# Performance work log

Hardware: AMD Instinct MI355X
Metric: run time of the kernel (lower is better)

The kernel has to match this reference:

```python
import jax, jax.numpy as jnp
import numpy as np

S, N, F, E, H = 64, 1000, 64, 128, 2  # seq_len, nodes/graph, node_dim, emb_dim, heads
DEG = 8
C = E // H  # per-head channels


def setup_inputs() -> dict:
    key = jax.random.key(0)
    ks = jax.random.split(key, 16)
    Ntot = S * N
    Eg = N * DEG
    src = jax.random.randint(ks[0], (S, Eg), 0, N)
    dst = jax.random.randint(ks[1], (S, Eg), 0, N)
    off = (jnp.arange(S) * N)[:, None]
    edge_index = jnp.stack([(src + off).reshape(-1), (dst + off).reshape(-1)]).astype(jnp.int32)
    nfm = jax.random.normal(ks[2], (Ntot, F), jnp.float32)
    reachable = jax.random.uniform(ks[3], (S, N)) > 0.2
    reachable = reachable.at[:, 0].set(True)  # ensure each row has a reachable node
    h0 = jnp.zeros((N, E), jnp.float32)
    c0 = jnp.zeros((N, E), jnp.float32)

    def lin(k, i, o):
        return (jax.random.normal(k, (i, o), jnp.float32) / np.sqrt(i)).astype(jnp.float32)

    return dict(
        nfm=nfm, edge_index=edge_index, reachable=reachable, h0=h0, c0=c0,
        gat_W1=lin(ks[4], F, E), gat_b1=jnp.zeros((E,), jnp.float32),
        gat_att1=(jax.random.normal(ks[5], (H, C), jnp.float32) / np.sqrt(C)).astype(jnp.float32),
        gat_bias1=jnp.zeros((E,), jnp.float32),
        gat_W=(jax.random.normal(ks[6], (4, E, E), jnp.float32) / np.sqrt(E)).astype(jnp.float32),
        gat_b=jnp.zeros((4, E), jnp.float32),
        gat_att=(jax.random.normal(ks[7], (4, H, C), jnp.float32) / np.sqrt(C)).astype(jnp.float32),
        gat_bias=jnp.zeros((4, E), jnp.float32),
        lstm_Wih=(jax.random.normal(ks[8], (4 * E, E), jnp.float32) / np.sqrt(E)).astype(jnp.float32),
        lstm_Whh=(jax.random.normal(ks[9], (4 * E, E), jnp.float32) / np.sqrt(E)).astype(jnp.float32),
        lstm_bih=jnp.zeros((4 * E,), jnp.float32), lstm_bhh=jnp.zeros((4 * E,), jnp.float32),
        th6_W=lin(ks[10], E, E), th6_b=jnp.zeros((E,), jnp.float32),
        th7_W=lin(ks[11], E, E), th7_b=jnp.zeros((E,), jnp.float32),
        th5_W=lin(ks[12], 2 * E, 1), th5_b=jnp.zeros((1,), jnp.float32),
    )


def _gat_layer(x, src, dst, W, b, att, bias, Ntot):
    # GATv2Conv, share_weights=True: x_l == x_r = lin(x)
    Hh, Ch = att.shape
    xl = (x @ W + b).reshape(-1, Hh, Ch)                 # [Ntot,H,C]
    e = jax.nn.leaky_relu(xl[src] + xl[dst], 0.2)        # [Etot,H,C]
    logit = jnp.einsum('ehc,hc->eh', e, att)             # [Etot,H]
    m = jax.ops.segment_max(logit, dst, num_segments=Ntot)
    a = jnp.exp(logit - m[dst])                          # segment-stable softmax
    denom = jax.ops.segment_sum(a, dst, num_segments=Ntot)
    alpha = a / denom[dst]
    out = jax.ops.segment_sum(xl[src] * alpha[:, :, None], dst, num_segments=Ntot)
    return out.reshape(-1, Hh * Ch) + bias               # concat heads + bias


def _forward(nfm, edge_index, reachable, h0, c0, gat_W1, gat_b1, gat_att1, gat_bias1,
             gat_W, gat_b, gat_att, gat_bias, lstm_Wih, lstm_Whh, lstm_bih, lstm_bhh,
             th6_W, th6_b, th7_W, th7_b, th5_W, th5_b):
    Ntot = nfm.shape[0]
    loops = jnp.arange(Ntot, dtype=edge_index.dtype)     # add_self_loops=True
    src = jnp.concatenate([edge_index[0], loops])
    dst = jnp.concatenate([edge_index[1], loops])

    x = jax.nn.relu(_gat_layer(nfm, src, dst, gat_W1, gat_b1, gat_att1, gat_bias1, Ntot))
    for i in range(4):  # layers 2..5; no activation after last
        x = _gat_layer(x, src, dst, gat_W[i], gat_b[i], gat_att[i], gat_bias[i], Ntot)
        if i < 3:
            x = jax.nn.relu(x)

    mu = x.reshape(S, N, E)                              # [seq, batch(=nodes), emb]

    def step(carry, xt):
        h, c = carry
        g = xt @ lstm_Wih.T + lstm_bih + h @ lstm_Whh.T + lstm_bhh
        i_, f_, gg, o_ = jnp.split(g, 4, axis=-1)        # torch gate order i,f,g,o
        c = jax.nn.sigmoid(f_) * c + jax.nn.sigmoid(i_) * jnp.tanh(gg)
        h = jax.nn.sigmoid(o_) * jnp.tanh(c)
        return (h, c), h

    (hT, cT), mu = jax.lax.scan(step, (h0, c0), mu)      # mu: [S,N,E]

    meanpool = mu.mean(axis=1, keepdims=True)            # [S,1,E]
    gs = meanpool @ th6_W + th6_b
    la = mu @ th7_W + th7_b
    rep = jax.nn.relu(jnp.concatenate([jnp.broadcast_to(gs, la.shape), la], axis=-1))
    logits = (rep @ th5_W)[..., 0] + th5_b               # [S,N]
    logits = jnp.where(reachable, logits, -jnp.inf)
    prob = jax.nn.softmax(logits, axis=1)
    return prob, hT, cT


def reference(nfm, edge_index, reachable, h0, c0, gat_W1, gat_b1, gat_att1, gat_bias1,
              gat_W, gat_b, gat_att, gat_bias, lstm_Wih, lstm_Whh, lstm_bih, lstm_bhh,
              th6_W, th6_b, th7_W, th7_b, th5_W, th5_b):
    return _forward(nfm, edge_index, reachable, h0, c0, gat_W1, gat_b1, gat_att1, gat_bias1,
                    gat_W, gat_b, gat_att, gat_bias, lstm_Wih, lstm_Whh, lstm_bih, lstm_bhh,
                    th6_W, th6_b, th7_W, th7_b, th5_W, th5_b)
```

## Files before the change

### kernel.cpp

```cpp
#include <hip/hip_runtime.h>
#include <hip/hip_bf16.h>

#define SQ   64
#define NN   1000
#define NT   64000
#define EE   128
#define EG   512000
#define ET   576000

#define WS_XA      0ull
#define WS_XB      33000000ull
#define WS_ROWPTR  66000000ull
#define WS_CURSOR  66300000ull
#define WS_SRCS    66600000ull
#define WS_INCL    69000000ull
#define WS_BSUM    69300000ull
#define WS_BOFF    69302048ull
#define WS_MODE    69304096ull
#define WS_WQA     70000000ull
#define WS_WQB     70262144ull
#define WS_AS      70600000ull
#define WS_LOGIT2  70700000ull
#define WS2_XC     33000000ull
#define WS2_BFRAG  164100000ull
#define WS2_GHI    164300000ull
#define WS2_GLO    164650000ull
#define WS2_B512   165000000ull
#define WS2_MODE   165010000ull
#define WS2_AS     165020000ull
#define WS2_LOGIT2 165100000ull
#define WS2_NEED   165360000ull
#define G_W1    0
#define G_WL    8192
#define G_PROJ  73728
#define G_W7    139264

typedef __attribute__((ext_vector_type(8))) short short8;
typedef __attribute__((ext_vector_type(4))) float f32x4;

__device__ __forceinline__ float rdlane(float v, int l) {
    return __int_as_float(__builtin_amdgcn_readlane(__float_as_int(v), l));
}
__device__ __forceinline__ float sigm(float x) { return 1.0f / (1.0f + __expf(-x)); }
__device__ __forceinline__ float tanh_f(float x) {
    x = fminf(fmaxf(x, -30.0f), 30.0f);
    float e = __expf(2.0f * x);
    return (e - 1.0f) / (e + 1.0f);
}
__device__ __forceinline__ float tanh2(float x) {
    return 2.0f / (1.0f + __expf(-2.0f * x)) - 1.0f;
}
__device__ __forceinline__ ushort f2bf(float x) {
    unsigned u = __float_as_uint(x);
    unsigned r = (u + 0x7FFFu + ((u >> 16) & 1u)) >> 16;
    return (ushort)r;
}
__device__ __forceinline__ float bf2f(ushort h) {
    return __uint_as_float(((unsigned)h) << 16);
}

__global__ void detect_mode_k(const unsigned char* __restrict__ p, int* __restrict__ mode) {
    __shared__ int f0, f3;
    const int t = threadIdx.x;
    if (t == 0) { f0 = 0; f3 = 0; }
    __syncthreads();
    int l0 = 0, l3 = 0;
    for (int i = t; i < 16000; i += 256) {
        if (p[4 * i])     l0 = 1;
        if (p[4 * i + 3]) l3 = 1;
    }
    if (l0) atomicOr(&f0, 1);
    if (l3) atomicOr(&f3, 1);
    __syncthreads();
    if (t == 0) {
        int m;
        if (f0 && f3)      m = 1;
        else if (f0)       m = 0;
        else               m = 2;
        *mode = m;
    }
}

__global__ void zero_ints_k(int* __restrict__ p, int n) {
    int i = blockIdx.x * 256 + threadIdx.x;
    if (i < n) p[i] = 0;
}
__global__ void hist_k(const int* __restrict__ ei, int* __restrict__ deg) {
    int e = blockIdx.x * 256 + threadIdx.x;
    if (e < ET) {
        int d = (e < EG) ? ei[EG + e] : (e - EG);
        atomicAdd(deg + d, 1);
    }
}
__global__ void scan1_k(const int* __restrict__ deg, int* __restrict__ incl, int* __restrict__ bsum) {
    __shared__ int sh[256];
    const int t = threadIdx.x;
    const int i = blockIdx.x * 256 + t;
    sh[t] = deg[i];
    __syncthreads();
    for (int o = 1; o < 256; o <<= 1) {
        int add = (t >= o) ? sh[t - o] : 0;
        __syncthreads();
        sh[t] += add;
        __syncthreads();
    }
    incl[i] = sh[t];
    if (t == 255) bsum[blockIdx.x] = sh[255];
}
__global__ void scan2_k(const int* __restrict__ bsum, int* __restrict__ boff) {
    __shared__ int sh[256];
    const int t = threadIdx.x;
    int v = (t < 250) ? bsum[t] : 0;
    sh[t] = v;
    __syncthreads();
    for (int o = 1; o < 256; o <<= 1) {
        int add = (t >= o) ? sh[t - o] : 0;
        __syncthreads();
        sh[t] += add;
        __syncthreads();
    }
    if (t < 250) boff[t] = sh[t] - v;
}
__global__ void scan3_k(const int* __restrict__ incl, const int* __restrict__ boff,
                        int* __restrict__ rowptr, int* __restrict__ cursor_deg) {
    const int i = blockIdx.x * 256 + threadIdx.x;
    int total = incl[i] + boff[blockIdx.x];
    int excl  = total - cursor_deg[i];
    rowptr[i] = excl;
    cursor_deg[i] = excl;
    if (i == NT - 1) rowptr[NT] = total;
}
__global__ void fill_k(const int* __restrict__ ei, int* __restrict__ cursor, int* __restrict__ srcs) {
    int e = blockIdx.x * 256 + threadIdx.x;
    if (e < ET) {
        int s_, d_;
        if (e < EG) { s_ = ei[e]; d_ = ei[EG + e]; }
        else        { s_ = e - EG; d_ = s_; }
        int p = atomicAdd(cursor + d_, 1);
        srcs[p] = s_;
    }
}

__global__ void build_gfrag_k(const float* __restrict__ src, const int ks, const int ns,
                              const int K, ushort* __restrict__ dhi, ushort* __restrict__ dlo,
                              const int total) {
    int id = blockIdx.x * 256 + threadIdx.x;
    if (id < total) {
        int j = id & 7, lane = (id >> 3) & 63;
        int f = id >> 9;
        int KT = K >> 5;
        int nt = f / KT, kt = f - nt * KT;
        int n = nt * 16 + (lane & 15);
        int k = kt * 32 + ((lane >> 4) << 3) + j;
        float v = src[(size_t)k * ks + (size_t)n * ns];
        ushort h = f2bf(v);
        dhi[id] = h;
        dlo[id] = f2bf(v - bf2f(h));
    }
}
__global__ void bias512_k(const float* __restrict__ bih, const float* __restrict__ bhh,
                          float* __restrict__ b512) {
    int i = blockIdx.x * 256 + threadIdx.x;
    if (i < 512) b512[i] = bih[i] + bhh[i];
}

template <int KT>
__global__ __launch_bounds__(256) void gemm_mf(
    const float* __restrict__ x, const ushort* __restrict__ bhi,
    const ushort* __restrict__ blo, const float* __restrict__ bias,
    float* __restrict__ out, const int ldout)
{
    constexpr int K = KT * 32;
    __shared__ __align__(16) ushort ahi_s[KT * 4 * 64 * 8];
    __shared__ __align__(16) ushort alo_s[KT * 4 * 64 * 8];
    const int t = threadIdx.x;
    const int w = t >> 6, lane = t & 63;
    const int quad = lane >> 4, col = lane & 15;
    const int row0 = blockIdx.x * 64;
    const int col0 = blockIdx.y * 128;

    {
        const int r  = t >> 2;
        const int kc = (t & 3) * (K / 4);
        const int rw = r >> 4, rcol = r & 15;
        const float* xr = x + (size_t)(row0 + r) * K + kc;
#pragma unroll
        for (int k = 0; k < K / 4; k += 4) {
            const int ch = kc + k;
            const int idx = (((ch >> 5) * 4 + rw) * 64 + ((ch >> 3) & 3) * 16 + rcol) * 8
                            + (ch & 7);
            float4 v = *(const float4*)(xr + k);
            ushort h0_ = f2bf(v.x), h1_ = f2bf(v.y), h2_ = f2bf(v.z), h3_ = f2bf(v.w);
            ushort l0_ = f2bf(v.x - bf2f(h0_)), l1_ = f2bf(v.y - bf2f(h1_));
            ushort l2_ = f2bf(v.z - bf2f(h2_)), l3_ = f2bf(v.w - bf2f(h3_));
            *(uint2*)(ahi_s + idx) = make_uint2((uint)h0_ | ((uint)h1_ << 16),
                                                (uint)h2_ | ((uint)h3_ << 16));
            *(uint2*)(alo_s + idx) = make_uint2((uint)l0_ | ((uint)l1_ << 16),
                                                (uint)l2_ | ((uint)l3_ << 16));
        }
    }
    __syncthreads();

    short8 ah[KT], al[KT];
#pragma unroll
    for (int kt = 0; kt < KT; kt++) {
        const int off = ((kt * 4 + w) * 64 + lane) * 8;
        ah[kt] = *(const short8*)(ahi_s + off);
        al[kt] = *(const short8*)(alo_s + off);
    }

    f32x4 acc[8];
#pragma unroll
    for (int q = 0; q < 8; q++) acc[q] = (f32x4){0.f, 0.f, 0.f, 0.f};

#pragma unroll
    for (int q = 0; q < 8; q++) {
#pragma unroll
        for (int kt = 0; kt < KT; kt++) {
            const int f = ((((col0 >> 4) + q) * KT + kt) * 64 + lane) * 8;
            short8 bh = *(const short8*)(bhi + f);
            short8 bl = *(const short8*)(blo + f);
            acc[q] = __builtin_amdgcn_mfma_f32_16x16x32_bf16(ah[kt], bh, acc[q], 0, 0, 0);
            acc[q] = __builtin_amdgcn_mfma_f32_16x16x32_bf16(al[kt], bh, acc[q], 0, 0, 0);
            acc[q] = __builtin_amdgcn_mfma_f32_16x16x32_bf16(ah[kt], bl, acc[q], 0, 0, 0);
        }
    }

#pragma unroll
    for (int q = 0; q < 8; q++) {
        float bv = bias[col0 + q * 16 + col];
#pragma unroll
        for (int r = 0; r < 4; r++) {
            out[(size_t)(row0 + w * 16 + quad * 4 + r) * ldout + col0 + q * 16 + col]
                = acc[q][r] + bv;
        }
    }
}

template <int K>
__global__ __launch_bounds__(256) void gemm3(
    const float* __restrict__ x, const float* __restrict__ W,
    const float* __restrict__ b, float* __restrict__ out)
{
    __shared__ float Wsh[64 * 128];
    __shared__ float xT[64][132];
    const int t = threadIdx.x;
    const int row0 = blockIdx.x * 128;
    const int cg = t & 15;
    const int rg = t >> 4;
    float4 acc[8][2];
#pragma unroll
    for (int r = 0; r < 8; r++) {
        acc[r][0] = make_float4(0.f, 0.f, 0.f, 0.f);
        acc[r][1] = make_float4(0.f, 0.f, 0.f, 0.f);
    }
    for (int k0 = 0; k0 < K; k0 += 64) {
        for (int i = t * 4; i < 64 * 128; i += 1024)
            *(float4*)(Wsh + i) = *(const float4*)(W + (size_t)k0 * 128 + i);
        for (int i = t * 4; i < 128 * 64; i += 1024) {
            int r = i >> 6, k = i & 63;
            float4 v = *(const float4*)(x + (size_t)(row0 + r) * K + k0 + k);
            xT[k + 0][r] = v.x; xT[k + 1][r] = v.y;
            xT[k + 2][r] = v.z; xT[k + 3][r] = v.w;
        }
        __syncthreads();
#pragma unroll 2
        for (int k = 0; k < 64; k++) {
            float4 w0 = *(const float4*)(Wsh + k * 128 + cg * 8);
            float4 w1 = *(const float4*)(Wsh + k * 128 + cg * 8 + 4);
            float4 x0 = *(const float4*)(&xT[k][rg * 8]);
            float4 x1 = *(const float4*)(&xT[k][rg * 8 + 4]);
            float xv[8] = {x0.x, x0.y, x0.z, x0.w, x1.x, x1.y, x1.z, x1.w};
#pragma unroll
            for (int r = 0; r < 8; r++) {
                acc[r][0].x += xv[r] * w0.x; acc[r][0].y += xv[r] * w0.y;
                acc[r][0].z += xv[r] * w0.z; acc[r][0].w += xv[r] * w0.w;
                acc[r][1].x += xv[r] * w1.x; acc[r][1].y += xv[r] * w1.y;
                acc[r][1].z += xv[r] * w1.z; acc[r][1].w += xv[r] * w1.w;
            }
        }
        __syncthreads();
    }
    float4 bv0 = *(const float4*)(b + cg * 8);
    float4 bv1 = *(const float4*)(b + cg * 8 + 4);
#pragma unroll
    for (int r = 0; r < 8; r++) {
        float4 o0, o1;
        o0.x = acc[r][0].x + bv0.x; o0.y = acc[r][0].y + bv0.y;
        o0.z = acc[r][0].z + bv0.z; o0.w = acc[r][0].w + bv0.w;
        o1.x = acc[r][1].x + bv1.x; o1.y = acc[r][1].y + bv1.y;
        o1.z = acc[r][1].z + bv1.z; o1.w = acc[r][1].w + bv1.w;
        float* op = out + (size_t)(row0 + rg * 8 + r) * 128 + cg * 8;
        *(float4*)(op) = o0;
        *(float4*)(op + 4) = o1;
    }
}

__global__ __launch_bounds__(256) void gat_fused_k(
    const float* __restrict__ xl, const int* __restrict__ rowptr,
    const int* __restrict__ srcs, const float* __restrict__ att,
    const float* __restrict__ bias, float* __restrict__ out, const int do_relu)
{
    const int lane = threadIdx.x & 63;
    const int q = lane & 31;
    const int h = lane >> 5;
    const int b = blockIdx.x;
    const int g = b & 7;
    const int j = b >> 3;
    const int jq = j / 250;
    const int jj = j - jq * 250;
    const int s = g + 8 * jq;
    const int n = s * NN + jj * 4 + (threadIdx.x >> 6);

    const float4 a4 = *(const float4*)(att + q * 4);
    const float4 xd = *(const float4*)(xl + (size_t)n * 128 + q * 4);
    const int i0 = rowptr[n], i1 = rowptr[n + 1];

    float m = -1e30f, d = 0.f;
    float ax = 0.f, ay = 0.f, az = 0.f, aw = 0.f;

    int i = i0 + h;
    int sv = (i < i1) ? srcs[i] : 0;
    for (int base = i0; base < i1; base += 2) {
        const bool valid = (i < i1);
        const int svn = (i + 2 < i1) ? srcs[i + 2] : 0;
        const float4 xs = *(const float4*)(xl + (size_t)sv * 128 + q * 4);
        float u0 = xs.x + xd.x, u1 = xs.y + xd.y;
        float u2 = xs.z + xd.z, u3 = xs.w + xd.w;
        float p;
        p  = a4.x * fmaxf(u0, 0.2f * u0);
        p += a4.y * fmaxf(u1, 0.2f * u1);
        p += a4.z * fmaxf(u2, 0.2f * u2);
        p += a4.w * fmaxf(u3, 0.2f * u3);
        p += __shfl_xor(p, 1);
        p += __shfl_xor(p, 2);
        p += __shfl_xor(p, 4);
        p += __shfl_xor(p, 8);
        float mn = fmaxf(m, valid ? p : -1e30f);
        float sc = __expf(m - mn);
        float wgt = valid ? __expf(p - mn) : 0.f;
        d  = d  * sc + wgt;
        ax = ax * sc + wgt * xs.x;
        ay = ay * sc + wgt * xs.y;
        az = az * sc + wgt * xs.z;
        aw = aw * sc + wgt * xs.w;
        m = mn;
        sv = svn;
        i += 2;
    }

    float m2 = __shfl_xor(m, 32);
    float d2 = __shfl_xor(d, 32);
    float bx = __shfl_xor(ax, 32);
    float by = __shfl_xor(ay, 32);
    float bz = __shfl_xor(az, 32);
    float bw = __shfl_xor(aw, 32);
    float mm = fmaxf(m, m2);
    float s1 = __expf(m - mm), s2 = __expf(m2 - mm);
    float den = d * s1 + d2 * s2;
    float inv = 1.f / den;
    float4 bv = *(const float4*)(bias + q * 4);
    float ox = (ax * s1 + bx * s2) * inv + bv.x;
    float oy = (ay * s1 + by * s2) * inv + bv.y;
    float oz = (az * s1 + bz * s2) * inv + bv.z;
    float ow = (aw * s1 + bw * s2) * inv + bv.w;
    if (do_relu) {
        ox = fmaxf(ox, 0.f); oy = fmaxf(oy, 0.f);
        oz = fmaxf(oz, 0.f); ow = fmaxf(ow, 0.f);
    }
    if (lane < 32)
        *(float4*)(out + (size_t)n * 128 + q * 4) = make_float4(ox, oy, oz, ow);
}

__global__ void build_wq_k(const float* __restrict__ Wih, const float* __restrict__ Whh,
                           float4* __restrict__ WQa, float4* __restrict__ WQb) {
    int id = blockIdx.x * 256 + threadIdx.x;
    if (id < 64 * 256) {
        int kp = id >> 8, t = id & 255;
        int j1 = t, j2 = t + 256;
        WQa[id] = make_float4(Wih[(size_t)j1 * 128 + 2 * kp], Whh[(size_t)j1 * 128 + 2 * kp],
                              Wih[(size_t)j1 * 128 + 2 * kp + 1], Whh[(size_t)j1 * 128 + 2 * kp + 1]);
        WQb[id] = make_float4(Wih[(size_t)j2 * 128 + 2 * kp], Whh[(size_t)j2 * 128 + 2 * kp],
                              Wih[(size_t)j2 * 128 + 2 * kp + 1], Whh[(size_t)j2 * 128 + 2 * kp + 1]);
    }
}

__global__ void build_bfrag_k(const float* __restrict__ Whh, ushort* __restrict__ Bfrag) {
    int id = blockIdx.x * 256 + threadIdx.x;
    if (id < 65536) {
        int j = id & 7, lane = (id >> 3) & 63, kt = (id >> 9) & 3, tile = id >> 11;
        int gate = tile * 16 + (lane & 15);
        int k = kt * 32 + ((lane >> 4) << 3) + j;
        Bfrag[id] = f2bf(Whh[(size_t)gate * 128 + k]);
    }
}

#define LSTM_GROUP(buf, gbase)                                                     \
    _Pragma("unroll")                                                              \
    for (int i_ = 0; i_ < 4; i_++) {                                               \
        const int kp_ = (gbase) * 4 + i_;                                          \
        const float4 qa_ = buf[i_];                                                \
        const float4 qb_ = buf[4 + i_];                                            \
        _Pragma("unroll")                                                          \
        for (int n_ = 0; n_ < 4; n_++) {                                           \
            const float sx0_ = rdlane(xr[n_].x, kp_);                              \
            const float sh0_ = rdlane(hr[n_].x, kp_);                              \
            const float sx1_ = rdlane(xr[n_].y, kp_);                              \
            const float sh1_ = rdlane(hr[n_].y, kp_);                              \
            acc1[n_] += sx0_ * qa_.x + sh0_ * qa_.y + sx1_ * qa_.z + sh1_ * qa_.w; \
            acc2[n_] += sx0_ * qb_.x + sh0_ * qb_.y + sx1_ * qb_.z + sh1_ * qb_.w; \
        }                                                                          \
    }

__global__ __launch_bounds__(256, 1) void lstm_k(
    float* __restrict__ mu, const float4* __restrict__ WQa, const float4* __restrict__ WQb,
    const float* __restrict__ bih, const float* __restrict__ bhh,
    const float* __restrict__ h0, const float* __restrict__ c0,
    float* __restrict__ hT, float* __restrict__ cT)
{
    const int t = threadIdx.x, lane = t & 63;
    const int n0 = blockIdx.x * 4;
    __shared__ float hsh[4][128];
    __shared__ float gsh[4][512];
    const float b1 = bih[t] + bhh[t];
    const float b2 = bih[t + 256] + bhh[t + 256];
    float creg[2];
#pragma unroll
    for (int q = 0; q < 2; q++) {
        int id = t + 256 * q;
        creg[q] = c0[(size_t)(n0 + (id >> 7)) * 128 + (id & 127)];
    }
    for (int i = t; i < 512; i += 256)
        hsh[i >> 7][i & 127] = h0[(size_t)(n0 + (i >> 7)) * 128 + (i & 127)];

    const float4* pA = WQa + t;
    const float4* pB = WQb + t;

    float2 xr[4], xnx[4];
#pragma unroll
    for (int n = 0; n < 4; n++)
        xr[n] = *(const float2*)(mu + (size_t)n0 * 128 + n * 128 + lane * 2);
    __syncthreads();

    for (int s = 0; s < SQ; s++) {
        float* xrow = mu + ((size_t)s * NN + n0) * 128;
        float2 hr[4];
#pragma unroll
        for (int n = 0; n < 4; n++) hr[n] = *(const float2*)(&hsh[n][lane * 2]);

        float4 bufA[8], bufB[8];
#pragma unroll
        for (int i = 0; i < 4; i++) { bufA[i] = pA[i * 256]; bufA[4 + i] = pB[i * 256]; }

        if (s + 1 < SQ) {
            const float* xrow2 = mu + ((size_t)(s + 1) * NN + n0) * 128;
#pragma unroll
            for (int n = 0; n < 4; n++) xnx[n] = *(const float2*)(xrow2 + n * 128 + lane * 2);
        }

        float acc1[4], acc2[4];
#pragma unroll
        for (int n = 0; n < 4; n++) { acc1[n] = b1; acc2[n] = b2; }

        for (int g = 0; g < 16; g += 2) {
#pragma unroll
            for (int i = 0; i < 4; i++) {
                bufB[i]     = pA[((g + 1) * 4 + i) * 256];
                bufB[4 + i] = pB[((g + 1) * 4 + i) * 256];
            }
            LSTM_GROUP(bufA, g)
            if (g < 14) {
#pragma unroll
                for (int i = 0; i < 4; i++) {
                    bufA[i]     = pA[((g + 2) * 4 + i) * 256];
                    bufA[4 + i] = pB[((g + 2) * 4 + i) * 256];
                }
            }
            LSTM_GROUP(bufB, g + 1)
        }

#pragma unroll
        for (int n = 0; n < 4; n++) { gsh[n][t] = acc1[n]; gsh[n][t + 256] = acc2[n]; }
        __syncthreads();
#pragma unroll
        for (int q = 0; q < 2; q++) {
            int id = t + 256 * q;
            int n = id >> 7, e = id & 127;
            float iv = gsh[n][e], fv = gsh[n][128 + e];
            float gv = gsh[n][256 + e], ov = gsh[n][384 + e];
            float c = sigm(fv) * creg[q] + sigm(iv) * tanh_f(gv);
            float h = sigm(ov) * tanh_f(c);
            creg[q] = c;
            hsh[n][e] = h;
            xrow[n * 128 + e] = h;
            if (s == SQ - 1) {
                hT[(size_t)(n0 + n) * 128 + e] = h;
                cT[(size_t)(n0 + n) * 128 + e] = c;
            }
        }
#pragma unroll
        for (int n = 0; n < 4; n++) xr[n] = xnx[n];
        __syncthreads();
    }
}

__global__ __launch_bounds__(512, 2) void lstm10_k(
    float* __restrict__ mu, const float* __restrict__ xC,
    const ushort* __restrict__ Bfrag,
    const float* __restrict__ h0, const float* __restrict__ c0,
    float* __restrict__ hT, float* __restrict__ cT)
{
    const int t = threadIdx.x;
    const int w = t >> 6, lane = t & 63;
    const int quad = lane >> 4;
    const int n0 = blockIdx.x * 4;
    const int enode = t >> 7;
    const int ech   = t & 127;

    __shared__ __align__(16) ushort hP[2][2][2048];
    __shared__ float gsh[4][512];

    short8 bf[4][4];
#pragma unroll
    for (int g4 = 0; g4 < 4; g4++)
#pragma unroll
        for (int kt = 0; kt < 4; kt++) {
            int tile = g4 * 8 + w;
            bf[g4][kt] = *(const short8*)(Bfrag + (((tile * 4 + kt) * 64 + lane) << 3));
        }

    const int epkt = ech >> 5, epqd = (ech >> 3) & 3, epj = ech & 7;
    const int epidx = epkt * 512 + (epqd * 16 + enode) * 8 + epj;

    for (int i = t; i < 2 * 2 * 2048; i += 512) ((ushort*)hP)[i] = 0;
    __syncthreads();
    {
        float v = h0[(size_t)(n0 + enode) * 128 + ech];
        ushort hh = f2bf(v), hl = f2bf(v - bf2f(hh));
        hP[0][0][epidx] = hh; hP[0][1][epidx] = hl;
        hP[1][0][epidx] = hh; hP[1][1][epidx] = hl;
    }
    float cst = c0[(size_t)(n0 + enode) * 128 + ech];

    float xcr[4], xcn[4];
#pragma unroll
    for (int g4 = 0; g4 < 4; g4++)
        xcr[g4] = xC[((size_t)(n0 + enode)) * 512 + g4 * 128 + ech];
    __syncthreads();

    int p = 0;
    for (int s = 0; s < SQ; s++) {
        if (s + 1 < SQ) {
            const float* xn = xC + ((size_t)(s + 1) * NN + n0 + enode) * 512;
#pragma unroll
            for (int g4 = 0; g4 < 4; g4++)
                xcn[g4] = xn[g4 * 128 + ech];
        }

        short8 ahi[4], alo[4];
#pragma unroll
        for (int kt = 0; kt < 4; kt++) {
            ahi[kt] = *(const short8*)(&hP[p][0][kt * 512 + lane * 8]);
            alo[kt] = *(const short8*)(&hP[p][1][kt * 512 + lane * 8]);
        }

        f32x4 acc[4];
#pragma unroll
        for (int g4 = 0; g4 < 4; g4++) acc[g4] = (f32x4){0.f, 0.f, 0.f, 0.f};
#pragma unroll
        for (int kt = 0; kt < 4; kt++) {
#pragma unroll
            for (int g4 = 0; g4 < 4; g4++)
                acc[g4] = __builtin_amdgcn_mfma_f32_16x16x32_bf16(ahi[kt], bf[g4][kt], acc[g4], 0, 0, 0);
#pragma unroll
            for (int g4 = 0; g4 < 4; g4++)
                acc[g4] = __builtin_amdgcn_mfma_f32_16x16x32_bf16(alo[kt], bf[g4][kt], acc[g4], 0, 0, 0);
        }

        if (quad == 0) {
            const int col = lane & 15;
#pragma unroll
            for (int g4 = 0; g4 < 4; g4++)
#pragma unroll
                for (int r = 0; r < 4; r++)
                    gsh[r][(g4 * 8 + w) * 16 + col] = acc[g4][r];
        }
        __syncthreads();

        {
            float iv = gsh[enode][0 * 128 + ech] + xcr[0];
            float fv = gsh[enode][1 * 128 + ech] + xcr[1];
            float gv = gsh[enode][2 * 128 + ech] + xcr[2];
            float ov = gsh[enode][3 * 128 + ech] + xcr[3];
            float c = sigm(fv) * cst + sigm(iv) * tanh2(gv);
            float h = sigm(ov) * tanh2(c);
            cst = c;
            const int pn = p ^ 1;
            ushort hh = f2bf(h);
            hP[pn][0][epidx] = hh;
            hP[pn][1][epidx] = f2bf(h - bf2f(hh));
            mu[((size_t)s * NN + n0 + enode) * 128 + ech] = h;
            if (s == SQ - 1) {
                hT[(size_t)(n0 + enode) * 128 + ech] = h;
                cT[(size_t)(n0 + enode) * 128 + ech] = c;
            }
            p = pn;
        }
#pragma unroll
        for (int g4 = 0; g4 < 4; g4++) xcr[g4] = xcn[g4];
        __syncthreads();
    }
}

__global__ __launch_bounds__(256) void meanpool_gs_k(
    const float* __restrict__ mu, const float* __restrict__ W6,
    const float* __restrict__ b6, const float* __restrict__ w5,
    float* __restrict__ A)
{
    const int s = blockIdx.x, t = threadIdx.x;
    const int ch = t & 127, half = t >> 7;
    __shared__ float mp[128];
    __shared__ float red[256];
    float acc = 0.f;
    for (int n = half * 500; n < (half + 1) * 500; n++)
        acc += mu[((size_t)s * NN + n) * 128 + ch];
    red[t] = acc;
    __syncthreads();
    if (t < 128) mp[t] = (red[t] + red[t + 128]) * 0.001f;
    __syncthreads();
    float g = 0.f;
    if (t < 128) {
        g = b6[t];
        for (int k = 0; k < 128; k++) g += mp[k] * W6[(size_t)k * 128 + t];
        g = fmaxf(g, 0.f) * w5[t];
    }
    red[t] = g;
    __syncthreads();
    for (int o = 128; o > 0; o >>= 1) {
        if (t < o) red[t] += red[t + o];
        __syncthreads();
    }
    if (t == 0) A[s] = red[0];
}

__global__ __launch_bounds__(256) void rowdot_k(
    const float* __restrict__ la, const float* __restrict__ w5,
    const float* __restrict__ b5, const float* __restrict__ A,
    float* __restrict__ out)
{
    const int lane = threadIdx.x & 63;
    const int row = blockIdx.x * 4 + (threadIdx.x >> 6);
    float2 v = *(const float2*)(la + (size_t)row * 128 + lane * 2);
    float2 w = *(const float2*)(w5 + 128 + lane * 2);
    float x = fmaxf(v.x, 0.f) * w.x + fmaxf(v.y, 0.f) * w.y;
#pragma unroll
    for (int o = 32; o; o >>= 1) x += __shfl_down(x, o);
    if (lane == 0) out[row] = x + A[row / NN] + b5[0];
}

__device__ __forceinline__ bool reach_at(const void* reach, int mode, int idx) {
    if (mode == 0) return ((const int*)reach)[idx] != 0;
    if (mode == 1) return ((const unsigned char*)reach)[idx] != 0;
    return ((const float*)reach)[idx] != 0.f;
}
__global__ __launch_bounds__(256) void softmax_k(
    const float* __restrict__ lg, const void* __restrict__ reach,
    const int* __restrict__ mode, float* __restrict__ prob)
{
    const int s = blockIdx.x, t = threadIdx.x;
    const int m = *mode;
    __shared__ float red[256];
    float mx = -1e30f;
    for (int i = t; i < NN; i += 256) {
        int idx = s * NN + i;
        if (reach_at(reach, m, idx)) mx = fmaxf(mx, lg[idx]);
    }
    red[t] = mx;
    __syncthreads();
    for (int o = 128; o; o >>= 1) {
        if (t < o) red[t] = fmaxf(red[t], red[t + o]);
        __syncthreads();
    }
    mx = red[0];
    __syncthreads();
    float sum = 0.f;
    for (int i = t; i < NN; i += 256) {
        int idx = s * NN + i;
        float v = reach_at(reach, m, idx) ? __expf(lg[idx] - mx) : 0.f;
        prob[idx] = v;
        sum += v;
    }
    red[t] = sum;
    __syncthreads();
    for (int o = 128; o; o >>= 1) {
        if (t < o) red[t] += red[t + o];
        __syncthreads();
    }
    float inv = 1.f / red[0];
    for (int i = t; i < NN; i += 256) prob[s * NN + i] *= inv;
}

extern "C" void kernel_launch(void* const* d_in, const int* in_sizes, int n_in,
                              void* d_out, int out_size, void* d_ws, size_t ws_size,
                              hipStream_t stream) {
    const float* nfm   = (const float*)d_in[0];
    const int*   ei    = (const int*)d_in[1];
    const void*  reach = d_in[2];
    const float* h0    = (const float*)d_in[3];
    const float* c0    = (const float*)d_in[4];
    const float* W1    = (const float*)d_in[5];
    const float* b1    = (const float*)d_in[6];
    const float* att1  = (const float*)d_in[7];
    const float* bias1 = (const float*)d_in[8];
    const float* Wl    = (const float*)d_in[9];
    const float* bl    = (const float*)d_in[10];
    const float* attl  = (const float*)d_in[11];
    const float* biasl = (const float*)d_in[12];
    const float* Wih   = (const float*)d_in[13];
    const float* Whh   = (const float*)d_in[14];
    const float* bih   = (const float*)d_in[15];
    const float* bhh   = (const float*)d_in[16];
    const float* W6    = (const float*)d_in[17];
    const float* b6    = (const float*)d_in[18];
    const float* W7    = (const float*)d_in[19];
    const float* b7    = (const float*)d_in[20];
    const float* w5    = (const float*)d_in[21];
    const float* b5    = (const float*)d_in[22];

    char* ws = (char*)d_ws;
    const bool bigws = (ws_size >= WS2_NEED);

    float*  xA     = (float*)(ws + WS_XA);
    float*  xB     = (float*)(ws + WS_XB);
    int*    rowptr = (int*)(ws + WS_ROWPTR);
    int*    cursor = (int*)(ws + WS_CURSOR);
    int*    srcs   = (int*)(ws + WS_SRCS);
    int*    incl   = (int*)(ws + WS_INCL);
    int*    bsum   = (int*)(ws + WS_BSUM);
    int*    boff   = (int*)(ws + WS_BOFF);
    int*    modep  = bigws ? (int*)(ws + WS2_MODE)     : (int*)(ws + WS_MODE);
    float*  As     = bigws ? (float*)(ws + WS2_AS)     : (float*)(ws + WS_AS);
    float*  logit2 = bigws ? (float*)(ws + WS2_LOGIT2) : (float*)(ws + WS_LOGIT2);
    float*  xC     = (float*)(ws + WS2_XC);
    ushort* Bfrag  = (ushort*)(ws + WS2_BFRAG);
    ushort* ghi    = (ushort*)(ws + WS2_GHI);
    ushort* glo    = (ushort*)(ws + WS2_GLO);
    float*  b512   = (float*)(ws + WS2_B512);
    float4* WQa    = (float4*)(ws + WS_WQA);
    float4* WQb    = (float4*)(ws + WS_WQB);

    float* prob = (float*)d_out;
    float* hT   = (float*)d_out + 64000;
    float* cT   = (float*)d_out + 192000;

    detect_mode_k<<<1, 256, 0, stream>>>((const unsigned char*)reach, modep);
    zero_ints_k<<<250, 256, 0, stream>>>(cursor, NT);
    hist_k<<<2250, 256, 0, stream>>>(ei, cursor);
    scan1_k<<<250, 256, 0, stream>>>(cursor, incl, bsum);
    scan2_k<<<1, 256, 0, stream>>>(bsum, boff);
    scan3_k<<<250, 256, 0, stream>>>(incl, boff, rowptr, cursor);
    fill_k<<<2250, 256, 0, stream>>>(ei, cursor, srcs);
    if (bigws) {
        build_bfrag_k<<<256, 256, 0, stream>>>(Whh, Bfrag);
        bias512_k<<<2, 256, 0, stream>>>(bih, bhh, b512);
        build_gfrag_k<<<32, 256, 0, stream>>>(W1, 128, 1, 64, ghi + G_W1, glo + G_W1, 8192);
        for (int i = 0; i < 4; i++)
            build_gfrag_k<<<64, 256, 0, stream>>>(Wl + (size_t)i * 16384, 128, 1, 128,
                                                  ghi + G_WL + i * 16384, glo + G_WL + i * 16384, 16384);
        build_gfrag_k<<<256, 256, 0, stream>>>(Wih, 1, 128, 128, ghi + G_PROJ, glo + G_PROJ, 65536);
        build_gfrag_k<<<64, 256, 0, stream>>>(W7, 128, 1, 128, ghi + G_W7, glo + G_W7, 16384);
    } else {
        build_wq_k<<<64, 256, 0, stream>>>(Wih, Whh, WQa, WQb);
    }

    for (int l = 0; l < 5; l++) {
        if (bigws) {
            if (l == 0)
                gemm_mf<2><<<dim3(1000, 1), 256, 0, stream>>>(nfm, ghi + G_W1, glo + G_W1, b1, xB, 128);
            else
                gemm_mf<4><<<dim3(1000, 1), 256, 0, stream>>>(xA, ghi + G_WL + (l - 1) * 16384,
                                                              glo + G_WL + (l - 1) * 16384,
                                                              bl + (l - 1) * 128, xB, 128);
        } else {
            if (l == 0)
                gemm3<64><<<500, 256, 0, stream>>>(nfm, W1, b1, xB);
            else
                gemm3<128><<<500, 256, 0, stream>>>(xA, Wl + (size_t)(l - 1) * 128 * 128,
                                                    bl + (l - 1) * 128, xB);
        }
        const float* att  = (l == 0) ? att1  : attl  + (l - 1) * 128;
        const float* bias = (l == 0) ? bias1 : biasl + (l - 1) * 128;
        gat_fused_k<<<16000, 256, 0, stream>>>(xB, rowptr, srcs, att, bias, xA,
                                               (l < 4) ? 1 : 0);
    }

    if (bigws) {
        gemm_mf<4><<<dim3(1000, 4), 256, 0, stream>>>(xA, ghi + G_PROJ, glo + G_PROJ, b512, xC, 512);
        lstm10_k<<<250, 512, 0, stream>>>(xA, xC, Bfrag, h0, c0, hT, cT);
    } else {
        lstm_k<<<250, 256, 0, stream>>>(xA, WQa, WQb, bih, bhh, h0, c0, hT, cT);
    }

    meanpool_gs_k<<<64, 256, 0, stream>>>(xA, W6, b6, w5, As);
    if (bigws)
        gemm_mf<4><<<dim3(1000, 1), 256, 0, stream>>>(xA, ghi + G_W7, glo + G_W7, b7, xB, 128);
    else
        gemm3<128><<<500, 256, 0, stream>>>(xA, W7, b7, xB);
    rowdot_k<<<16000, 256, 0, stream>>>(xB, w5, b5, As, logit2);
    softmax_k<<<64, 256, 0, stream>>>(logit2, reach, modep, prob);
}
```

Before: 692.9 us.

## Merge weight-prep launches, dual-stream GAT edge loop, pad LSTM h buffer

Nine small weight-preparation kernels become one launch that picks its task from the block index, which cuts launch overhead. The GAT aggregation loop now runs two independent online-softmax streams per half-wave, with two edges' source loads in flight and merged at the end, to hide gather latency. The LSTM kernel keeps h in a padded row-major shared buffer (stride 136) instead of a fragment-ordered layout, which changes the LDS access pattern and zero-pads the unused rows. The cost is more registers in the GAT kernel and a more irregular LDS read pattern in the LSTM.

```diff
diff --git a/kernel.cpp b/kernel.cpp
--- a/kernel.cpp
+++ b/kernel.cpp
@@ -141,10 +141,10 @@
     }
 }
 
-__global__ void build_gfrag_k(const float* __restrict__ src, const int ks, const int ns,
-                              const int K, ushort* __restrict__ dhi, ushort* __restrict__ dlo,
-                              const int total) {
-    int id = blockIdx.x * 256 + threadIdx.x;
+__device__ __forceinline__ void gfrag_dev(const float* __restrict__ src, const int ks,
+                                          const int ns, const int K,
+                                          ushort* __restrict__ dhi, ushort* __restrict__ dlo,
+                                          const int total, const int id) {
     if (id < total) {
         int j = id & 7, lane = (id >> 3) & 63;
         int f = id >> 9;
@@ -158,10 +158,34 @@
         dlo[id] = f2bf(v - bf2f(h));
     }
 }
-__global__ void bias512_k(const float* __restrict__ bih, const float* __restrict__ bhh,
-                          float* __restrict__ b512) {
-    int i = blockIdx.x * 256 + threadIdx.x;
-    if (i < 512) b512[i] = bih[i] + bhh[i];
+__global__ void build_all_k(const float* __restrict__ Whh, const float* __restrict__ bih,
+                            const float* __restrict__ bhh, const float* __restrict__ W1,
+                            const float* __restrict__ Wl, const float* __restrict__ Wih,
+                            const float* __restrict__ W7, ushort* __restrict__ Bfrag,
+                            float* __restrict__ b512, ushort* __restrict__ ghi,
+                            ushort* __restrict__ glo) {
+    const int b = blockIdx.x, t = threadIdx.x;
+    if (b < 256) {
+        int id = b * 256 + t;
+        int j = id & 7, lane = (id >> 3) & 63, kt = (id >> 9) & 3, tile = id >> 11;
+        int gate = tile * 16 + (lane & 15);
+        int k = kt * 32 + ((lane >> 4) << 3) + j;
+        Bfrag[id] = f2bf(Whh[(size_t)gate * 128 + k]);
+    } else if (b < 258) {
+        int i = (b - 256) * 256 + t;
+        if (i < 512) b512[i] = bih[i] + bhh[i];
+    } else if (b < 290) {
+        gfrag_dev(W1, 128, 1, 64, ghi + G_W1, glo + G_W1, 8192, (b - 258) * 256 + t);
+    } else if (b < 546) {
+        int bb = b - 290;
+        int i = bb >> 6;
+        gfrag_dev(Wl + (size_t)i * 16384, 128, 1, 128,
+                  ghi + G_WL + i * 16384, glo + G_WL + i * 16384, 16384, (bb & 63) * 256 + t);
+    } else if (b < 802) {
+        gfrag_dev(Wih, 1, 128, 128, ghi + G_PROJ, glo + G_PROJ, 65536, (b - 546) * 256 + t);
+    } else {
+        gfrag_dev(W7, 128, 1, 128, ghi + G_W7, glo + G_W7, 16384, (b - 802) * 256 + t);
+    }
 }
 
 template <int KT>
@@ -316,38 +340,63 @@
     const float4 xd = *(const float4*)(xl + (size_t)n * 128 + q * 4);
     const int i0 = rowptr[n], i1 = rowptr[n + 1];
 
-    float m = -1e30f, d = 0.f;
-    float ax = 0.f, ay = 0.f, az = 0.f, aw = 0.f;
-
-    int i = i0 + h;
-    int sv = (i < i1) ? srcs[i] : 0;
-    for (int base = i0; base < i1; base += 2) {
-        const bool valid = (i < i1);
-        const int svn = (i + 2 < i1) ? srcs[i + 2] : 0;
-        const float4 xs = *(const float4*)(xl + (size_t)sv * 128 + q * 4);
-        float u0 = xs.x + xd.x, u1 = xs.y + xd.y;
-        float u2 = xs.z + xd.z, u3 = xs.w + xd.w;
-        float p;
-        p  = a4.x * fmaxf(u0, 0.2f * u0);
-        p += a4.y * fmaxf(u1, 0.2f * u1);
-        p += a4.z * fmaxf(u2, 0.2f * u2);
-        p += a4.w * fmaxf(u3, 0.2f * u3);
-        p += __shfl_xor(p, 1);
-        p += __shfl_xor(p, 2);
-        p += __shfl_xor(p, 4);
-        p += __shfl_xor(p, 8);
-        float mn = fmaxf(m, valid ? p : -1e30f);
-        float sc = __expf(m - mn);
-        float wgt = valid ? __expf(p - mn) : 0.f;
-        d  = d  * sc + wgt;
-        ax = ax * sc + wgt * xs.x;
-        ay = ay * sc + wgt * xs.y;
-        az = az * sc + wgt * xs.z;
-        aw = aw * sc + wgt * xs.w;
-        m = mn;
-        sv = svn;
-        i += 2;
-    }
+    float mA = -1e30f, dA = 0.f, axA = 0.f, ayA = 0.f, azA = 0.f, awA = 0.f;
+    float mB = -1e30f, dB = 0.f, axB = 0.f, ayB = 0.f, azB = 0.f, awB = 0.f;
+
+    int iA = i0 + h, iB = i0 + h + 2;
+    int svA = (iA < i1) ? srcs[iA] : 0;
+    int svB = (iB < i1) ? srcs[iB] : 0;
+    float4 xsA = *(const float4*)(xl + (size_t)svA * 128 + q * 4);
+    float4 xsB = *(const float4*)(xl + (size_t)svB * 128 + q * 4);
+
+    for (int base = i0; base < i1; base += 4) {
+        const bool vA = (iA < i1), vB = (iB < i1);
+        const int svA2 = (iA + 4 < i1) ? srcs[iA + 4] : 0;
+        const int svB2 = (iB + 4 < i1) ? srcs[iB + 4] : 0;
+        const float4 xA2 = *(const float4*)(xl + (size_t)svA2 * 128 + q * 4);
+        const float4 xB2 = *(const float4*)(xl + (size_t)svB2 * 128 + q * 4);
+
+        float uA0 = xsA.x + xd.x, uA1 = xsA.y + xd.y;
+        float uA2 = xsA.z + xd.z, uA3 = xsA.w + xd.w;
+        float uB0 = xsB.x + xd.x, uB1 = xsB.y + xd.y;
+        float uB2 = xsB.z + xd.z, uB3 = xsB.w + xd.w;
+        float pA, pB;
+        pA  = a4.x * fmaxf(uA0, 0.2f * uA0);
+        pA += a4.y * fmaxf(uA1, 0.2f * uA1);
+        pA += a4.z * fmaxf(uA2, 0.2f * uA2);
+        pA += a4.w * fmaxf(uA3, 0.2f * uA3);
+        pB  = a4.x * fmaxf(uB0, 0.2f * uB0);
+        pB += a4.y * fmaxf(uB1, 0.2f * uB1);
+        pB += a4.z * fmaxf(uB2, 0.2f * uB2);
+        pB += a4.w * fmaxf(uB3, 0.2f * uB3);
+        pA += __shfl_xor(pA, 1);   pB += __shfl_xor(pB, 1);
+        pA += __shfl_xor(pA, 2);   pB += __shfl_xor(pB, 2);
+        pA += __shfl_xor(pA, 4);   pB += __shfl_xor(pB, 4);
+        pA += __shfl_xor(pA, 8);   pB += __shfl_xor(pB, 8);
+
+        float mnA = fmaxf(mA, vA ? pA : -1e30f);
+        float mnB = fmaxf(mB, vB ? pB : -1e30f);
+        float scA = __expf(mA - mnA), scB = __expf(mB - mnB);
+        float wA = vA ? __expf(pA - mnA) : 0.f;
+        float wB = vB ? __expf(pB - mnB) : 0.f;
+        dA  = dA  * scA + wA;          dB  = dB  * scB + wB;
+        axA = axA * scA + wA * xsA.x;  axB = axB * scB + wB * xsB.x;
+        ayA = ayA * scA + wA * xsA.y;  ayB = ayB * scB + wB * xsB.y;
+        azA = azA * scA + wA * xsA.z;  azB = azB * scB + wB * xsB.z;
+        awA = awA * scA + wA * xsA.w;  awB = awB * scB + wB * xsB.w;
+        mA = mnA; mB = mnB;
+        xsA = xA2; xsB = xB2;
+        iA += 4; iB += 4;
+    }
+
+    float m1 = fmaxf(mA, mB);
+    float sA = __expf(mA - m1), sB = __expf(mB - m1);
+    float d  = dA * sA + dB * sB;
+    float ax = axA * sA + axB * sB;
+    float ay = ayA * sA + ayB * sB;
+    float az = azA * sA + azB * sB;
+    float aw = awA * sA + awB * sB;
+    float m  = m1;
 
     float m2 = __shfl_xor(m, 32);
     float d2 = __shfl_xor(d, 32);
@@ -385,16 +434,6 @@
     }
 }
 
-__global__ void build_bfrag_k(const float* __restrict__ Whh, ushort* __restrict__ Bfrag) {
-    int id = blockIdx.x * 256 + threadIdx.x;
-    if (id < 65536) {
-        int j = id & 7, lane = (id >> 3) & 63, kt = (id >> 9) & 3, tile = id >> 11;
-        int gate = tile * 16 + (lane & 15);
-        int k = kt * 32 + ((lane >> 4) << 3) + j;
-        Bfrag[id] = f2bf(Whh[(size_t)gate * 128 + k]);
-    }
-}
-
 #define LSTM_GROUP(buf, gbase)                                                     \
     _Pragma("unroll")                                                              \
     for (int i_ = 0; i_ < 4; i_++) {                                               \
@@ -504,7 +543,7 @@
     }
 }
 
-__global__ __launch_bounds__(512, 2) void lstm10_k(
+__global__ __launch_bounds__(512, 2) void lstm8_k(
     float* __restrict__ mu, const float* __restrict__ xC,
     const ushort* __restrict__ Bfrag,
     const float* __restrict__ h0, const float* __restrict__ c0,
@@ -512,12 +551,12 @@
 {
     const int t = threadIdx.x;
     const int w = t >> 6, lane = t & 63;
-    const int quad = lane >> 4;
+    const int quad = lane >> 4, col = lane & 15;
     const int n0 = blockIdx.x * 4;
     const int enode = t >> 7;
     const int ech   = t & 127;
 
-    __shared__ __align__(16) ushort hP[2][2][2048];
+    __shared__ __align__(16) ushort hbuf[2][2][16 * 136];
     __shared__ float gsh[4][512];
 
     short8 bf[4][4];
@@ -529,16 +568,12 @@
             bf[g4][kt] = *(const short8*)(Bfrag + (((tile * 4 + kt) * 64 + lane) << 3));
         }
 
-    const int epkt = ech >> 5, epqd = (ech >> 3) & 3, epj = ech & 7;
-    const int epidx = epkt * 512 + (epqd * 16 + enode) * 8 + epj;
-
-    for (int i = t; i < 2 * 2 * 2048; i += 512) ((ushort*)hP)[i] = 0;
-    __syncthreads();
-    {
-        float v = h0[(size_t)(n0 + enode) * 128 + ech];
+    for (int i = t; i < 2048; i += 512) {
+        int node = i >> 7, ee = i & 127;
+        float v = (node < 4) ? h0[(size_t)(n0 + node) * 128 + ee] : 0.f;
         ushort hh = f2bf(v), hl = f2bf(v - bf2f(hh));
-        hP[0][0][epidx] = hh; hP[0][1][epidx] = hl;
-        hP[1][0][epidx] = hh; hP[1][1][epidx] = hl;
+        hbuf[0][0][node * 136 + ee] = hh; hbuf[0][1][node * 136 + ee] = hl;
+        hbuf[1][0][node * 136 + ee] = hh; hbuf[1][1][node * 136 + ee] = hl;
     }
     float cst = c0[(size_t)(n0 + enode) * 128 + ech];
 
@@ -560,8 +595,8 @@
         short8 ahi[4], alo[4];
 #pragma unroll
         for (int kt = 0; kt < 4; kt++) {
-            ahi[kt] = *(const short8*)(&hP[p][0][kt * 512 + lane * 8]);
-            alo[kt] = *(const short8*)(&hP[p][1][kt * 512 + lane * 8]);
+            ahi[kt] = *(const short8*)(&hbuf[p][0][col * 136 + kt * 32 + quad * 8]);
+            alo[kt] = *(const short8*)(&hbuf[p][1][col * 136 + kt * 32 + quad * 8]);
         }
 
         f32x4 acc[4];
@@ -578,7 +613,6 @@
         }
 
         if (quad == 0) {
-            const int col = lane & 15;
 #pragma unroll
             for (int g4 = 0; g4 < 4; g4++)
 #pragma unroll
@@ -597,8 +631,8 @@
             cst = c;
             const int pn = p ^ 1;
             ushort hh = f2bf(h);
-            hP[pn][0][epidx] = hh;
-            hP[pn][1][epidx] = f2bf(h - bf2f(hh));
+            hbuf[pn][0][enode * 136 + ech] = hh;
+            hbuf[pn][1][enode * 136 + ech] = f2bf(h - bf2f(hh));
             mu[((size_t)s * NN + n0 + enode) * 128 + ech] = h;
             if (s == SQ - 1) {
                 hT[(size_t)(n0 + enode) * 128 + ech] = h;
@@ -761,14 +795,8 @@
     scan3_k<<<250, 256, 0, stream>>>(incl, boff, rowptr, cursor);
     fill_k<<<2250, 256, 0, stream>>>(ei, cursor, srcs);
     if (bigws) {
-        build_bfrag_k<<<256, 256, 0, stream>>>(Whh, Bfrag);
-        bias512_k<<<2, 256, 0, stream>>>(bih, bhh, b512);
-        build_gfrag_k<<<32, 256, 0, stream>>>(W1, 128, 1, 64, ghi + G_W1, glo + G_W1, 8192);
-        for (int i = 0; i < 4; i++)
-            build_gfrag_k<<<64, 256, 0, stream>>>(Wl + (size_t)i * 16384, 128, 1, 128,
-                                                  ghi + G_WL + i * 16384, glo + G_WL + i * 16384, 16384);
-        build_gfrag_k<<<256, 256, 0, stream>>>(Wih, 1, 128, 128, ghi + G_PROJ, glo + G_PROJ, 65536);
-        build_gfrag_k<<<64, 256, 0, stream>>>(W7, 128, 1, 128, ghi + G_W7, glo + G_W7, 16384);
+        build_all_k<<<866, 256, 0, stream>>>(Whh, bih, bhh, W1, Wl, Wih, W7,
+                                             Bfrag, b512, ghi, glo);
     } else {
         build_wq_k<<<64, 256, 0, stream>>>(Wih, Whh, WQa, WQb);
     }
@@ -796,7 +824,7 @@
 
     if (bigws) {
         gemm_mf<4><<<dim3(1000, 4), 256, 0, stream>>>(xA, ghi + G_PROJ, glo + G_PROJ, b512, xC, 512);
-        lstm10_k<<<250, 512, 0, stream>>>(xA, xC, Bfrag, h0, c0, hT, cT);
+        lstm8_k<<<250, 512, 0, stream>>>(xA, xC, Bfrag, h0, c0, hT, cT);
     } else {
         lstm_k<<<250, 256, 0, stream>>>(xA, WQa, WQb, bih, bhh, h0, c0, hT, cT);
     }
```

New measurement: 667.3 us. 1.04x faster.
